# Performance work log

Hardware: AMD Instinct MI355X
Metric: run time of the kernel (lower is better)

The kernel has to match this reference:

```python
import jax, jax.numpy as jnp
import numpy as np

G = 2      # num_generations
B = 16     # meta batch
N = 128    # num_sample
D = 128    # node feature dim (= base_c)
BASE = 128
H = 8      # mha heads
DK = 16    # mha d_k (H*DK = D)
BN_EPS = 1e-5


def setup_inputs() -> dict:
    key = jax.random.key(0)
    ks = jax.random.split(key, 18)

    def nrm(k, shp, s=0.05):
        return jax.random.normal(k, shp, dtype=jnp.float32) * s

    return {
        "vp": jax.random.normal(ks[0], (B, N, D), dtype=jnp.float32),
        "ep": jax.random.uniform(ks[1], (B, N, N), dtype=jnp.float32),
        "ps_w1": nrm(ks[2], (G, 2 * BASE, D)),
        "ps_g1": 1.0 + nrm(ks[3], (G, 2 * BASE), 0.1),
        "ps_b1": nrm(ks[4], (G, 2 * BASE), 0.1),
        "ps_w2": nrm(ks[5], (G, BASE, 2 * BASE)),
        "ps_g2": 1.0 + nrm(ks[6], (G, BASE), 0.1),
        "ps_b2": nrm(ks[7], (G, BASE), 0.1),
        "ps_w3": nrm(ks[8], (G, 1, BASE)),
        "ps_b3": nrm(ks[9], (G, 1), 0.1),
        "d2p_w1": nrm(ks[10], (G, 2 * BASE, 2 * D)),
        "d2p_g1": 1.0 + nrm(ks[11], (G, 2 * BASE), 0.1),
        "d2p_b1": nrm(ks[12], (G, 2 * BASE), 0.1),
        "d2p_w2": nrm(ks[13], (G, BASE, 2 * BASE)),
        "d2p_g2": 1.0 + nrm(ks[14], (G, BASE), 0.1),
        "d2p_b2": nrm(ks[15], (G, BASE), 0.1),
        "wq": nrm(ks[16], (G, H * DK, D)),
        "wk": nrm(ks[17], (G, H * DK, D)),
    }


def _bn(x, g, b):
    # eval-mode BatchNorm with default running stats (mean=0, var=1)
    return x * (g / jnp.sqrt(1.0 + BN_EPS)) + b


def _lrelu(x):
    return jnp.where(x >= 0, x, 0.01 * x)


def _l1norm(x):
    # torch F.normalize(p=1, dim=-1)
    return x / jnp.maximum(jnp.sum(jnp.abs(x), -1, keepdims=True), 1e-12)


def _point_sim(vp, ep, w1, g1, b1, w2, g2, b2, w3, b3, layer):
    # vp: [B,N,D]  ep: [B,N,N]; l2 distance metric
    diff = (vp[:, :, None, :] - vp[:, None, :, :]) ** 2          # [B,N,N,D]
    h = _lrelu(_bn(jnp.einsum('bijd,cd->bijc', diff, w1), g1, b1))  # [B,N,N,2*BASE]
    h = _lrelu(_bn(jnp.einsum('bijc,ec->bije', h, w2), g2, b2))     # [B,N,N,BASE]
    s = jax.nn.sigmoid(jnp.einsum('bije,oe->bijo', h, w3) + b3)[..., 0]  # [B,N,N]
    eye = jnp.eye(N, dtype=vp.dtype)
    ep0 = ep * (1.0 - eye)
    ep_sum = jnp.sum(ep0, -1, keepdims=True)
    e = s * ep0
    if layer > 0:  # PointSimilarity2: top-k sparsify (reproduces torch scatter on dim 1)
        ratio = 0.1 * layer
        kval = int(N * (1.0 - ratio))
        _, idx = jax.lax.top_k(e, kval)                          # [B,N,kval], over dim 2
        bb = jnp.arange(B)[:, None, None]
        kk = jnp.arange(kval)[None, None, :]
        mask = jnp.zeros((B, N, N), dtype=e.dtype).at[bb, idx, kk].set(1.0)
        e = e * mask
    e = _l1norm(e) * ep_sum
    e = e + eye + 1e-6
    e = e / jnp.sum(e, -1, keepdims=True)
    node_sim = -jnp.sum(diff, -1)                                 # [B,N,N]
    return e, node_sim


def _mha_attn(x, wq_g, wk_g):
    # attention-matrix-only MHA; average over heads -> [B,N,N]
    q = (x @ wq_g.T).reshape(B, N, H, DK)
    k = (x @ wk_g.T).reshape(B, N, H, DK)
    logits = jnp.einsum('bihd,bjhd->bhij', q, k) / np.sqrt(DK).astype(np.float32)
    return jnp.mean(jax.nn.softmax(logits, axis=-1), axis=1)


def _d2p(edge, vp, w1, g1, b1, w2, g2, b2):
    eye = jnp.eye(N, dtype=vp.dtype)
    e = _l1norm(edge * (1.0 - eye))
    aggr = jnp.einsum('bij,bjd->bid', e, vp)                      # bmm
    feat = jnp.concatenate([vp, aggr], -1)                        # [B,N,2D]
    h = _lrelu(_bn(feat @ w1.T, g1, b1))
    h = _lrelu(_bn(h @ w2.T, g2, b2))
    return h


def reference(vp, ep, ps_w1, ps_g1, ps_b1, ps_w2, ps_g2, ps_b2, ps_w3, ps_b3,
              d2p_w1, d2p_g1, d2p_b1, d2p_w2, d2p_g2, d2p_b2, wq, wk):
    eps_out, sims_out = [], []
    for g in range(G):
        e, ns = _point_sim(vp, ep, ps_w1[g], ps_g1[g], ps_b1[g], ps_w2[g], ps_g2[g],
                           ps_b2[g], ps_w3[g], ps_b3[g], layer=g)
        attn = _mha_attn(vp, wq[g], wk[g])
        e_fused = 0.5 * (e + attn)
        vp = _d2p(e_fused, vp, d2p_w1[g], d2p_g1[g], d2p_b1[g], d2p_w2[g], d2p_g2[g], d2p_b2[g])
        ep = e
        eps_out.append(e)
        sims_out.append(ns)
    return jnp.stack(eps_out), jnp.stack(sims_out), vp
```

## Files before the change

### kernel.cpp

```cpp
#include <hip/hip_runtime.h>
#include <hip/hip_bf16.h>

typedef unsigned int u32;
typedef unsigned short u16;
typedef float f32x4 __attribute__((ext_vector_type(4)));
typedef float f32x16 __attribute__((ext_vector_type(16)));
typedef short bh8 __attribute__((ext_vector_type(8)));

#define NB 16
#define NN 128
#define DD 128

__device__ __forceinline__ u16 f2bf(float f) {
  union { float f; u32 u; } x; x.f = f;
  u32 r = (x.u + 0x7fffu + ((x.u >> 16) & 1u)) >> 16;
  return (u16)r;
}
__device__ __forceinline__ float bf2f(u16 h) {
  union { u32 u; float f; } x; x.u = ((u32)h) << 16;
  return x.f;
}
__device__ __forceinline__ float lrelu(float x) { return x >= 0.f ? x : 0.01f * x; }
__device__ __forceinline__ f32x16 zero16() {
  f32x16 v;
  #pragma unroll
  for (int r = 0; r < 16; ++r) v[r] = 0.f;
  return v;
}

__global__ void k_pack(const float* __restrict__ ps_w1, const float* __restrict__ ps_w2,
                       const float* __restrict__ d2p_w1, const float* __restrict__ d2p_w2,
                       const float* __restrict__ wq, const float* __restrict__ wk,
                       u16* __restrict__ w1p, u16* __restrict__ w2p,
                       u16* __restrict__ wqA, u16* __restrict__ wkA,
                       u16* __restrict__ w1A, u16* __restrict__ w2A)
{
  int idx = blockIdx.x * 256 + threadIdx.x;
  if (idx < 65536) {
    int r = idx & 7, lane = (idx >> 3) & 63, f = (idx >> 9) & 63, g = idx >> 15;
    int ct = f >> 3, ks = f & 7;
    int c = ct * 32 + (lane & 31), d = ks * 16 + (lane >> 5) * 8 + r;
    w1p[idx] = f2bf(ps_w1[(size_t)g * 32768 + c * 128 + d]);
    return;
  }
  idx -= 65536;
  if (idx < 65536) {
    int r = idx & 7, lane = (idx >> 3) & 63, f = (idx >> 9) & 63, g = idx >> 15;
    int et = f >> 4, ks2 = f & 15;
    int e = et * 32 + (lane & 31), c = ks2 * 16 + (lane >> 5) * 8 + r;
    w2p[idx] = f2bf(ps_w2[(size_t)g * 32768 + e * 256 + c]);
    return;
  }
  idx -= 65536;
  if (idx < 32768) {
    int r = idx & 7, lane = (idx >> 3) & 63, ks = (idx >> 9) & 7, ot = (idx >> 12) & 3, g = idx >> 14;
    int o = ot * 32 + (lane & 31), d = ks * 16 + (lane >> 5) * 8 + r;
    wqA[idx] = f2bf(wq[(size_t)g * 16384 + o * 128 + d]);
    return;
  }
  idx -= 32768;
  if (idx < 32768) {
    int r = idx & 7, lane = (idx >> 3) & 63, ks = (idx >> 9) & 7, ot = (idx >> 12) & 3, g = idx >> 14;
    int o = ot * 32 + (lane & 31), d = ks * 16 + (lane >> 5) * 8 + r;
    wkA[idx] = f2bf(wk[(size_t)g * 16384 + o * 128 + d]);
    return;
  }
  idx -= 32768;
  if (idx < 131072) {
    int r = idx & 7, lane = (idx >> 3) & 63, ks = (idx >> 9) & 15, ot = (idx >> 13) & 7, g = idx >> 16;
    int o = ot * 32 + (lane & 31), q = ks * 16 + (lane >> 5) * 8 + r;
    w1A[idx] = f2bf(d2p_w1[(size_t)g * 65536 + o * 256 + q]);
    return;
  }
  idx -= 131072;
  if (idx < 65536) {
    int r = idx & 7, lane = (idx >> 3) & 63, ks = (idx >> 9) & 15, ot = (idx >> 13) & 3, g = idx >> 15;
    int o = ot * 32 + (lane & 31), q = ks * 16 + (lane >> 5) * 8 + r;
    w2A[idx] = f2bf(d2p_w2[(size_t)g * 32768 + o * 256 + q]);
    return;
  }
}

__global__ __launch_bounds__(256, 2)
void k_point_sim(const float* __restrict__ vp,
                 const u16* __restrict__ w1p, const u16* __restrict__ w2p,
                 const float* __restrict__ g1v, const float* __restrict__ b1v,
                 const float* __restrict__ g2v, const float* __restrict__ b2v,
                 const float* __restrict__ w3v, const float* __restrict__ b3v,
                 float* __restrict__ s_out, float* __restrict__ sims_out)
{
  const int bid = blockIdx.x;
  const int half = bid & 1;
  int rem = (bid >> 1) % 36;
  const int b = (bid >> 1) / 36;
  int ti = 0;
  while (rem >= 8 - ti) { rem -= 8 - ti; ++ti; }
  const int tj = ti + rem;

  const int t = threadIdx.x;
  const int lane = t & 63;
  const int w = t >> 6;
  const int p_l = lane & 31;
  const int hi = lane >> 5;
  const float rsbn = rsqrtf(1.0f + 1e-5f);

  __shared__ u16 Adiff[2][32 * 128];
  __shared__ u16 HL[2][32 * 256];
  __shared__ float sc1[256], bb1[256];
  __shared__ float sc2[128], bb2[128], w3s[128];
  __shared__ float sred[2][4][32];
  __shared__ float simv[128], svv[128];

  sc1[t] = g1v[t] * rsbn; bb1[t] = b1v[t];
  if (t < 128) { sc2[t] = g2v[t] * rsbn; bb2[t] = b2v[t]; w3s[t] = w3v[t]; }

  bh8 a1[2][8];
  #pragma unroll
  for (int c2 = 0; c2 < 2; ++c2)
    #pragma unroll
    for (int ks = 0; ks < 8; ++ks)
      a1[c2][ks] = *(const bh8*)(w1p + (((w * 2 + c2) * 8 + ks) * 64 + lane) * 8);
  bh8 a2[16];
  #pragma unroll
  for (int ks = 0; ks < 16; ++ks)
    a2[ks] = *(const bh8*)(w2p + ((w * 16 + ks) * 64 + lane) * 8);

  const int mtA = half * 4;
  const float* vpb = vp + (size_t)b * NN * DD;

  auto diffgen = [&](int mt, int buf) {
    int p = t >> 3, dseg = t & 7;
    int il = mt * 2 + (p >> 4), jl = p & 15;
    int i = ti * 16 + il, j = tj * 16 + jl;
    const float4* vi = (const float4*)(vpb + i * DD + dseg * 16);
    const float4* vj = (const float4*)(vpb + j * DD + dseg * 16);
    float rs = 0.f;
    u32 pw[8];
    #pragma unroll
    for (int c = 0; c < 4; ++c) {
      float4 av = vi[c], bv = vj[c];
      float d0 = av.x - bv.x; d0 *= d0;
      float d1 = av.y - bv.y; d1 *= d1;
      float d2 = av.z - bv.z; d2 *= d2;
      float d3 = av.w - bv.w; d3 *= d3;
      rs += d0 + d1 + d2 + d3;
      pw[c * 2]     = (u32)f2bf(d0) | ((u32)f2bf(d1) << 16);
      pw[c * 2 + 1] = (u32)f2bf(d2) | ((u32)f2bf(d3) << 16);
    }
    int base = p * 256;
    int off0 = (dseg * 32) ^ ((p & 15) << 4);
    int off1 = (dseg * 32 + 16) ^ ((p & 15) << 4);
    uint4 q0; q0.x = pw[0]; q0.y = pw[1]; q0.z = pw[2]; q0.w = pw[3];
    uint4 q1; q1.x = pw[4]; q1.y = pw[5]; q1.z = pw[6]; q1.w = pw[7];
    *(uint4*)((char*)Adiff[buf] + base + off0) = q0;
    *(uint4*)((char*)Adiff[buf] + base + off1) = q1;
    rs += __shfl_xor(rs, 1);
    rs += __shfl_xor(rs, 2);
    rs += __shfl_xor(rs, 4);
    if ((t & 7) == 0) simv[(mt - mtA) * 32 + p] = rs;
  };

  auto do_l2 = [&](int src) {
    f32x16 acc2 = zero16();
    #pragma unroll
    for (int ks2 = 0; ks2 < 16; ++ks2) {
      int byte = p_l * 512 + ((ks2 * 32 + hi * 16) ^ (p_l << 4));
      bh8 bf = *(const bh8*)((const char*)HL[src] + byte);
      acc2 = __builtin_amdgcn_mfma_f32_32x32x16_bf16(a2[ks2], bf, acc2, 0, 0, 0);
    }
    float psum = 0.f;
    #pragma unroll
    for (int r = 0; r < 16; ++r) {
      int e = w * 32 + (r & 3) + 8 * (r >> 2) + 4 * hi;
      float v = lrelu(acc2[r] * sc2[e] + bb2[e]);
      psum += v * w3s[e];
    }
    psum += __shfl_xor(psum, 32);
    if (hi == 0) sred[src][w][p_l] = psum;
  };

  auto s_final = [&](int ml) {
    if (t < 32) {
      float z = sred[ml & 1][0][t] + sred[ml & 1][1][t] + sred[ml & 1][2][t]
              + sred[ml & 1][3][t] + b3v[0];
      svv[ml * 32 + t] = 1.f / (1.f + __expf(-z));
    }
  };

  diffgen(mtA, 0);
  __syncthreads();

  #pragma unroll
  for (int m = 0; m < 4; ++m) {
    const int cur = m & 1;
    f32x16 acc1[2];
    acc1[0] = zero16(); acc1[1] = zero16();
    #pragma unroll
    for (int ks = 0; ks < 8; ++ks) {
      int byte = p_l * 256 + ((ks * 32 + hi * 16) ^ ((p_l & 15) << 4));
      bh8 bf = *(const bh8*)((const char*)Adiff[cur] + byte);
      acc1[0] = __builtin_amdgcn_mfma_f32_32x32x16_bf16(a1[0][ks], bf, acc1[0], 0, 0, 0);
      acc1[1] = __builtin_amdgcn_mfma_f32_32x32x16_bf16(a1[1][ks], bf, acc1[1], 0, 0, 0);
    }
    if (m < 3) diffgen(mtA + m + 1, cur ^ 1);
    if (m > 0) do_l2(cur ^ 1);
    if (m >= 2) s_final(m - 2);
    #pragma unroll
    for (int c2 = 0; c2 < 2; ++c2) {
      #pragma unroll
      for (int g4 = 0; g4 < 4; ++g4) {
        int c0 = (w * 2 + c2) * 32 + g4 * 8 + hi * 4;
        float v0 = lrelu(acc1[c2][g4 * 4 + 0] * sc1[c0 + 0] + bb1[c0 + 0]);
        float v1 = lrelu(acc1[c2][g4 * 4 + 1] * sc1[c0 + 1] + bb1[c0 + 1]);
        float v2 = lrelu(acc1[c2][g4 * 4 + 2] * sc1[c0 + 2] + bb1[c0 + 2]);
        float v3 = lrelu(acc1[c2][g4 * 4 + 3] * sc1[c0 + 3] + bb1[c0 + 3]);
        uint2 pk;
        pk.x = (u32)f2bf(v0) | ((u32)f2bf(v1) << 16);
        pk.y = (u32)f2bf(v2) | ((u32)f2bf(v3) << 16);
        int byte = p_l * 512 + ((c0 * 2) ^ (p_l << 4));
        *(uint2*)((char*)HL[cur] + byte) = pk;
      }
    }
    __syncthreads();
  }
  do_l2(1);
  s_final(2);
  __syncthreads();
  s_final(3);
  __syncthreads();

  {
    int idx = t & 127;
    int mm = idx >> 5, pp = idx & 31;
    int mt = mtA + mm;
    int i = ti * 16 + mt * 2 + (pp >> 4);
    int j = tj * 16 + (pp & 15);
    float sv = svv[idx];
    float sm = -simv[idx];
    if (t < 128) {
      s_out[(size_t)(b * NN + i) * NN + j] = sv;
      sims_out[(size_t)(b * NN + i) * NN + j] = sm;
    } else if (ti != tj) {
      s_out[(size_t)(b * NN + j) * NN + i] = sv;
      sims_out[(size_t)(b * NN + j) * NN + i] = sm;
    }
  }
}

__global__ void k_rank(const float* __restrict__ s_buf, const float* __restrict__ ep_prev,
                       float* __restrict__ mask)
{
  const int b = blockIdx.x >> 7, n = blockIdx.x & 127, t = threadIdx.x;
  __shared__ float ev[NN];
  size_t row = (size_t)(b * NN + n) * NN;
  float v = s_buf[row + t] * ((t == n) ? 0.f : ep_prev[row + t]);
  ev[t] = v;
  __syncthreads();
  int r = 0;
  for (int j = 0; j < NN; ++j) {
    float vj = ev[j];
    r += (vj > v) || (vj == v && j < t);
  }
  if (r < 115) mask[(size_t)(b * NN + t) * NN + r] = 1.0f;
}

__global__ __launch_bounds__(256)
void k_edge_prep(const float* __restrict__ s_buf, const float* __restrict__ ep_prev,
                 float* __restrict__ maskb, int use_mask, float* __restrict__ eps_out,
                 const float* __restrict__ vp,
                 const u16* __restrict__ wqA, const u16* __restrict__ wkA,
                 u16* __restrict__ Qb, u16* __restrict__ Kb,
                 u16* __restrict__ VPb, u16* __restrict__ VPT)
{
  __shared__ char shm[8448];
  const int t = threadIdx.x;

  if (blockIdx.x < 1024) {
    float* red  = (float*)shm;
    float* red2 = (float*)shm + 8;
    const int rr = t >> 7, tl = t & 127;
    const int rowid = blockIdx.x * 2 + rr;
    const int i = rowid & 127;
    const int wl = (t >> 6) & 1;
    size_t row = (size_t)rowid * 128;
    float ep0 = (tl == i) ? 0.f : ep_prev[row + tl];
    float e = s_buf[row + tl] * ep0;
    if (use_mask) e *= maskb[row + tl];
    else maskb[row + tl] = 0.f;
    float a = ep0, c = fabsf(e);
    #pragma unroll
    for (int o = 32; o; o >>= 1) { a += __shfl_xor(a, o); c += __shfl_xor(c, o); }
    if ((t & 63) == 0) { red[(rr * 2 + wl) * 2 + 0] = a; red[(rr * 2 + wl) * 2 + 1] = c; }
    __syncthreads();
    float epsum = red[(rr * 2) * 2] + red[(rr * 2 + 1) * 2];
    float l1 = red[(rr * 2) * 2 + 1] + red[(rr * 2 + 1) * 2 + 1];
    e = e / fmaxf(l1, 1e-12f) * epsum;
    e += ((tl == i) ? 1.f : 0.f) + 1e-6f;
    float d = e;
    #pragma unroll
    for (int o = 32; o; o >>= 1) d += __shfl_xor(d, o);
    if ((t & 63) == 0) red2[rr * 2 + wl] = d;
    __syncthreads();
    eps_out[row + tl] = e / (red2[rr * 2] + red2[rr * 2 + 1]);
    return;
  }

  u16* VPs = (u16*)shm;
  const int pb = blockIdx.x - 1024;
  const int b = pb >> 2, nt = pb & 3;
  const int w = t >> 6, lane = t & 63, l31 = lane & 31, hi = lane >> 5;
  const float* vpb = vp + (size_t)b * 16384 + (size_t)nt * 32 * 128;

  {
    int r = t >> 3, cseg = t & 7;
    float v[16];
    const float4* src = (const float4*)(vpb + r * 128 + cseg * 16);
    #pragma unroll
    for (int c = 0; c < 4; ++c) {
      float4 a = src[c];
      v[c * 4 + 0] = a.x; v[c * 4 + 1] = a.y; v[c * 4 + 2] = a.z; v[c * 4 + 3] = a.w;
    }
    uint4 pk0, pk1;
    u32* p0 = (u32*)&pk0; u32* p1 = (u32*)&pk1;
    #pragma unroll
    for (int k = 0; k < 4; ++k) {
      p0[k] = (u32)f2bf(v[k * 2 + 0]) | ((u32)f2bf(v[k * 2 + 1]) << 16);
      p1[k] = (u32)f2bf(v[8 + k * 2 + 0]) | ((u32)f2bf(v[8 + k * 2 + 1]) << 16);
    }
    u16* vb = VPb + (size_t)b * 16384 + (nt * 32 + r) * 128 + cseg * 16;
    *(uint4*)(vb) = pk0;
    *(uint4*)(vb + 8) = pk1;
    *(uint4*)((char*)VPs + r * 256 + ((cseg * 32) ^ ((r & 15) << 4))) = pk0;
    *(uint4*)((char*)VPs + r * 256 + ((cseg * 32 + 16) ^ ((r & 15) << 4))) = pk1;
  }
  __syncthreads();

  {
    int col = t >> 1, hh = t & 1;
    u16 tmp[16];
    #pragma unroll
    for (int rr2 = 0; rr2 < 16; ++rr2) {
      int row = hh * 16 + rr2;
      tmp[rr2] = *(const u16*)((char*)VPs + row * 256 + ((col * 2) ^ ((row & 15) << 4)));
    }
    *(uint4*)(VPT + (size_t)b * 16384 + col * 128 + nt * 32 + hh * 16) = *(uint4*)&tmp[0];
    *(uint4*)(VPT + (size_t)b * 16384 + col * 128 + nt * 32 + hh * 16 + 8) = *(uint4*)&tmp[8];
  }

  {
    const int isK = w >> 1;
    const int otp = (w & 1) * 2;
    const u16* wA = isK ? wkA : wqA;
    u16* DST = (isK ? Kb : Qb) + (size_t)b * 16384;
    bh8 bf[8];
    #pragma unroll
    for (int ks = 0; ks < 8; ++ks)
      bf[ks] = *(const bh8*)((char*)VPs + l31 * 256 + (((ks * 32) + hi * 16) ^ ((l31 & 15) << 4)));
    #pragma unroll
    for (int oo = 0; oo < 2; ++oo) {
      int ot = otp + oo;
      f32x16 acc = zero16();
      #pragma unroll
      for (int ks = 0; ks < 8; ++ks) {
        bh8 af = *(const bh8*)(wA + ((size_t)(ot * 8 + ks) * 64 + lane) * 8);
        acc = __builtin_amdgcn_mfma_f32_32x32x16_bf16(af, bf[ks], acc, 0, 0, 0);
      }
      int n = nt * 32 + l31;
      #pragma unroll
      for (int q4 = 0; q4 < 4; ++q4) {
        int o0 = ot * 32 + q4 * 8 + hi * 4;
        uint2 pk;
        pk.x = (u32)f2bf(acc[q4 * 4 + 0]) | ((u32)f2bf(acc[q4 * 4 + 1]) << 16);
        pk.y = (u32)f2bf(acc[q4 * 4 + 2]) | ((u32)f2bf(acc[q4 * 4 + 3]) << 16);
        *(uint2*)(DST + n * 128 + o0) = pk;
      }
    }
  }
}

__global__ __launch_bounds__(256)
void k_attn_d2p(const u16* __restrict__ Qb, const u16* __restrict__ Kb,
                const float* __restrict__ eps_g,
                const u16* __restrict__ VPb, const u16* __restrict__ VPT,
                const u16* __restrict__ w1A, const float* __restrict__ g1v, const float* __restrict__ b1v,
                const u16* __restrict__ w2A, const float* __restrict__ g2v, const float* __restrict__ b2v,
                float* __restrict__ vpn)
{
  __shared__ char shm[40960];
  u16* att  = (u16*)shm;
  u16* AG   = (u16*)shm;
  u16* HB   = (u16*)(shm + 8192);
  u16* EFNl = (u16*)(shm + 32768);

  const int b = blockIdx.x >> 2;
  const int ch = blockIdx.x & 3;
  const int t = threadIdx.x;
  const int w = t >> 6;
  const int lane = t & 63;
  const int l31 = lane & 31;
  const int hi = lane >> 5;
  const float rsbn = rsqrtf(1.f + 1e-5f);

  {
    float asum[64];
    #pragma unroll
    for (int z = 0; z < 64; ++z) asum[z] = 0.f;
    const u16* Qrow = Qb + (size_t)b * 16384 + (ch * 32 + l31) * 128;
    #pragma unroll
    for (int hh = 0; hh < 2; ++hh) {
      int h = w * 2 + hh;
      bh8 qf = *(const bh8*)(Qrow + h * 16 + hi * 8);
      f32x16 lg[4];
      #pragma unroll
      for (int jt = 0; jt < 4; ++jt) {
        bh8 kf = *(const bh8*)(Kb + (size_t)b * 16384 + (jt * 32 + l31) * 128 + h * 16 + hi * 8);
        f32x16 zz = zero16();
        lg[jt] = __builtin_amdgcn_mfma_f32_32x32x16_bf16(kf, qf, zz, 0, 0, 0);
      }
      float m = lg[0][0];
      #pragma unroll
      for (int jt = 0; jt < 4; ++jt)
        #pragma unroll
        for (int r = 0; r < 16; ++r) m = fmaxf(m, lg[jt][r]);
      m = fmaxf(m, __shfl_xor(m, 32));
      float sum = 0.f;
      #pragma unroll
      for (int jt = 0; jt < 4; ++jt)
        #pragma unroll
        for (int r = 0; r < 16; ++r) {
          float e = __expf((lg[jt][r] - m) * 0.25f);
          lg[jt][r] = e;
          sum += e;
        }
      sum += __shfl_xor(sum, 32);
      float inv = 1.f / sum;
      #pragma unroll
      for (int jt = 0; jt < 4; ++jt)
        #pragma unroll
        for (int r = 0; r < 16; ++r) asum[jt * 16 + r] += lg[jt][r] * inv;
    }
    #pragma unroll
    for (int jt = 0; jt < 4; ++jt)
      #pragma unroll
      for (int q4 = 0; q4 < 4; ++q4) {
        int j0 = jt * 32 + q4 * 8 + hi * 4;
        uint2 pk;
        pk.x = (u32)f2bf(asum[jt * 16 + q4 * 4 + 0]) | ((u32)f2bf(asum[jt * 16 + q4 * 4 + 1]) << 16);
        pk.y = (u32)f2bf(asum[jt * 16 + q4 * 4 + 2]) | ((u32)f2bf(asum[jt * 16 + q4 * 4 + 3]) << 16);
        *(uint2*)((char*)att + (w * 32 + l31) * 256 + ((j0 * 2) ^ ((l31 & 15) << 4))) = pk;
      }
  }
  __syncthreads();

  {
    int il = t >> 3, jseg = t & 7;
    int i = ch * 32 + il;
    float a[16];
    #pragma unroll
    for (int z = 0; z < 16; ++z) a[z] = 0.f;
    #pragma unroll
    for (int ww = 0; ww < 4; ++ww) {
      #pragma unroll
      for (int c = 0; c < 2; ++c) {
        uint4 v = *(const uint4*)((char*)att + (ww * 32 + il) * 256 + (((jseg * 32) + c * 16) ^ ((il & 15) << 4)));
        u32 uu[4] = {v.x, v.y, v.z, v.w};
        #pragma unroll
        for (int k = 0; k < 4; ++k) {
          a[c * 8 + k * 2 + 0] += bf2f((u16)(uu[k] & 0xffff));
          a[c * 8 + k * 2 + 1] += bf2f((u16)(uu[k] >> 16));
        }
      }
    }
    const float* erow = eps_g + ((size_t)b * 128 + i) * 128 + jseg * 16;
    float f[16];
    float s = 0.f;
    #pragma unroll
    for (int c = 0; c < 4; ++c) {
      float4 ev = *(const float4*)(erow + c * 4);
      float evs[4] = {ev.x, ev.y, ev.z, ev.w};
      #pragma unroll
      for (int k = 0; k < 4; ++k) {
        int jj = jseg * 16 + c * 4 + k;
        float fv = 0.5f * (evs[k] + a[c * 4 + k] * 0.125f);
        if (jj == i) fv = 0.f;
        f[c * 4 + k] = fv;
        s += fabsf(fv);
      }
    }
    s += __shfl_xor(s, 1);
    s += __shfl_xor(s, 2);
    s += __shfl_xor(s, 4);
    float inv = 1.f / fmaxf(s, 1e-12f);
    uint4 o0, o1;
    u32* op = (u32*)&o0;
    u32* op1 = (u32*)&o1;
    #pragma unroll
    for (int k = 0; k < 4; ++k) {
      op[k]  = (u32)f2bf(f[k * 2 + 0] * inv) | ((u32)f2bf(f[k * 2 + 1] * inv) << 16);
      op1[k] = (u32)f2bf(f[8 + k * 2 + 0] * inv) | ((u32)f2bf(f[8 + k * 2 + 1] * inv) << 16);
    }
    __syncthreads();
    *(uint4*)((char*)EFNl + il * 256 + ((jseg * 32) ^ ((il & 15) << 4))) = o0;
    *(uint4*)((char*)EFNl + il * 256 + ((jseg * 32 + 16) ^ ((il & 15) << 4))) = o1;
  }
  __syncthreads();

  {
    const u16* vtrow = VPT + (size_t)b * 16384 + (w * 32 + l31) * 128;
    f32x16 acc = zero16();
    #pragma unroll
    for (int ks = 0; ks < 8; ++ks) {
      bh8 af = *(const bh8*)(vtrow + ks * 16 + hi * 8);
      bh8 bf = *(const bh8*)((char*)EFNl + l31 * 256 + (((ks * 32) + hi * 16) ^ ((l31 & 15) << 4)));
      acc = __builtin_amdgcn_mfma_f32_32x32x16_bf16(af, bf, acc, 0, 0, 0);
    }
    #pragma unroll
    for (int q4 = 0; q4 < 4; ++q4) {
      int d0 = w * 32 + q4 * 8 + hi * 4;
      uint2 pk;
      pk.x = (u32)f2bf(acc[q4 * 4 + 0]) | ((u32)f2bf(acc[q4 * 4 + 1]) << 16);
      pk.y = (u32)f2bf(acc[q4 * 4 + 2]) | ((u32)f2bf(acc[q4 * 4 + 3]) << 16);
      *(uint2*)((char*)AG + l31 * 256 + ((d0 * 2) ^ ((l31 & 15) << 4))) = pk;
    }
  }
  __syncthreads();

  {
    const u16* vprow = VPb + (size_t)b * 16384 + (ch * 32 + l31) * 128;
    f32x16 acc0 = zero16(), acc1v = zero16();
    #pragma unroll
    for (int ks = 0; ks < 16; ++ks) {
      bh8 a0 = *(const bh8*)(w1A + ((size_t)((w * 2 + 0) * 16 + ks)) * 512 + lane * 8);
      bh8 a1 = *(const bh8*)(w1A + ((size_t)((w * 2 + 1) * 16 + ks)) * 512 + lane * 8);
      bh8 bf;
      if (ks < 8) bf = *(const bh8*)(vprow + ks * 16 + hi * 8);
      else bf = *(const bh8*)((char*)AG + l31 * 256 + ((((ks - 8) * 32) + hi * 16) ^ ((l31 & 15) << 4)));
      acc0 = __builtin_amdgcn_mfma_f32_32x32x16_bf16(a0, bf, acc0, 0, 0, 0);
      acc1v = __builtin_amdgcn_mfma_f32_32x32x16_bf16(a1, bf, acc1v, 0, 0, 0);
    }
    #pragma unroll
    for (int oo = 0; oo < 2; ++oo) {
      const f32x16& acc = oo ? acc1v : acc0;
      #pragma unroll
      for (int q4 = 0; q4 < 4; ++q4) {
        int o0 = (w * 2 + oo) * 32 + q4 * 8 + hi * 4;
        float4 gg = *(const float4*)(g1v + o0);
        float4 bb = *(const float4*)(b1v + o0);
        float v0 = lrelu(acc[q4 * 4 + 0] * (gg.x * rsbn) + bb.x);
        float v1 = lrelu(acc[q4 * 4 + 1] * (gg.y * rsbn) + bb.y);
        float v2 = lrelu(acc[q4 * 4 + 2] * (gg.z * rsbn) + bb.z);
        float v3 = lrelu(acc[q4 * 4 + 3] * (gg.w * rsbn) + bb.w);
        uint2 pk;
        pk.x = (u32)f2bf(v0) | ((u32)f2bf(v1) << 16);
        pk.y = (u32)f2bf(v2) | ((u32)f2bf(v3) << 16);
        *(uint2*)((char*)HB + l31 * 512 + ((o0 * 2) ^ (l31 << 4))) = pk;
      }
    }
  }
  __syncthreads();

  {
    f32x16 acc = zero16();
    #pragma unroll
    for (int ks = 0; ks < 16; ++ks) {
      bh8 af = *(const bh8*)(w2A + ((size_t)(w * 16 + ks)) * 512 + lane * 8);
      bh8 bf = *(const bh8*)((char*)HB + l31 * 512 + (((ks * 32) + hi * 16) ^ (l31 << 4)));
      acc = __builtin_amdgcn_mfma_f32_32x32x16_bf16(af, bf, acc, 0, 0, 0);
    }
    int i = ch * 32 + l31;
    #pragma unroll
    for (int q4 = 0; q4 < 4; ++q4) {
      int o0 = w * 32 + q4 * 8 + hi * 4;
      float4 gg = *(const float4*)(g2v + o0);
      float4 bb = *(const float4*)(b2v + o0);
      float4 ov;
      ov.x = lrelu(acc[q4 * 4 + 0] * (gg.x * rsbn) + bb.x);
      ov.y = lrelu(acc[q4 * 4 + 1] * (gg.y * rsbn) + bb.y);
      ov.z = lrelu(acc[q4 * 4 + 2] * (gg.z * rsbn) + bb.z);
      ov.w = lrelu(acc[q4 * 4 + 3] * (gg.w * rsbn) + bb.w);
      *(float4*)(vpn + ((size_t)b * 128 + i) * 128 + o0) = ov;
    }
  }
}

extern "C" void kernel_launch(void* const* d_in, const int* in_sizes, int n_in,
                              void* d_out, int out_size, void* d_ws, size_t ws_size,
                              hipStream_t stream)
{
  (void)in_sizes; (void)n_in; (void)out_size; (void)ws_size;
  const float* vp_in  = (const float*)d_in[0];
  const float* ep_in  = (const float*)d_in[1];
  const float* ps_w1  = (const float*)d_in[2];
  const float* ps_g1  = (const float*)d_in[3];
  const float* ps_b1  = (const float*)d_in[4];
  const float* ps_w2  = (const float*)d_in[5];
  const float* ps_g2  = (const float*)d_in[6];
  const float* ps_b2  = (const float*)d_in[7];
  const float* ps_w3  = (const float*)d_in[8];
  const float* ps_b3  = (const float*)d_in[9];
  const float* d2p_w1 = (const float*)d_in[10];
  const float* d2p_g1 = (const float*)d_in[11];
  const float* d2p_b1 = (const float*)d_in[12];
  const float* d2p_w2 = (const float*)d_in[13];
  const float* d2p_g2 = (const float*)d_in[14];
  const float* d2p_b2 = (const float*)d_in[15];
  const float* wq     = (const float*)d_in[16];
  const float* wk     = (const float*)d_in[17];

  float* out = (float*)d_out;
  float* eps_base  = out;
  float* sims_base = out + 524288;
  float* vp_out    = out + 1048576;

  char* ws = (char*)d_ws;
  float* s_buf = (float*)(ws + ((size_t)0 << 20));
  float* maskb = (float*)(ws + ((size_t)1 << 20));
  float* vp1   = (float*)(ws + ((size_t)2 << 20));
  u16* Qb   = (u16*)(ws + ((size_t)3 << 20));
  u16* Kb   = (u16*)(ws + ((size_t)3 << 20) + 524288);
  u16* VPb  = (u16*)(ws + ((size_t)4 << 20));
  u16* VPT  = (u16*)(ws + ((size_t)4 << 20) + 524288);
  u16* w1p  = (u16*)(ws + ((size_t)5 << 20));
  u16* w2p  = w1p + 65536;
  u16* wqA  = w2p + 65536;
  u16* wkA  = wqA + 32768;
  u16* w1A  = wkA + 32768;
  u16* w2A  = w1A + 131072;

  k_pack<<<dim3(1536), 256, 0, stream>>>(ps_w1, ps_w2, d2p_w1, d2p_w2, wq, wk,
                                         w1p, w2p, wqA, wkA, w1A, w2A);

  for (int g = 0; g < 2; ++g) {
    const float* vpc = g ? (const float*)vp1 : vp_in;
    float* vpn = g ? vp_out : vp1;
    float* eps_g  = eps_base + (size_t)g * 262144;
    float* sims_g = sims_base + (size_t)g * 262144;
    const float* epprev = g ? eps_base : ep_in;

    k_point_sim<<<dim3(1152), 256, 0, stream>>>(vpc,
        w1p + (size_t)g * 32768, w2p + (size_t)g * 32768,
        ps_g1 + g * 256, ps_b1 + g * 256,
        ps_g2 + g * 128, ps_b2 + g * 128,
        ps_w3 + g * 128, ps_b3 + g, s_buf, sims_g);
    if (g) k_rank<<<dim3(2048), 128, 0, stream>>>(s_buf, epprev, maskb);
    k_edge_prep<<<dim3(1088), 256, 0, stream>>>(s_buf, epprev, maskb, g, eps_g,
        vpc, wqA + (size_t)g * 16384, wkA + (size_t)g * 16384, Qb, Kb, VPb, VPT);
    k_attn_d2p<<<dim3(64), 256, 0, stream>>>(Qb, Kb, eps_g, VPb, VPT,
        w1A + (size_t)g * 65536, d2p_g1 + g * 256, d2p_b1 + g * 256,
        w2A + (size_t)g * 32768, d2p_g2 + g * 128, d2p_b2 + g * 128, vpn);
  }
}
```

Measured before the change: 135.7 us.

## Use hardware bf16 pack conversion, branchless lrelu, direct output stores, higher occupancy

Replaces the software round-to-nearest bf16 packing with the v_cvt_pk_bf16_f32 instruction in every kernel, and rewrites leaky ReLU as a max. This cuts ALU work in the epilogues. In the point-similarity kernel the staging arrays for sims and sigmoid outputs are removed: values are written straight to global memory, which drops a barrier and some LDS use. The launch bound is raised to three blocks per CU, which may force register spills given the large A-fragment register cache.

```diff
diff --git a/kernel.cpp b/kernel.cpp
--- a/kernel.cpp
+++ b/kernel.cpp
@@ -16,11 +16,16 @@
   u32 r = (x.u + 0x7fffu + ((x.u >> 16) & 1u)) >> 16;
   return (u16)r;
 }
+__device__ __forceinline__ u32 cvtpk(float lo, float hi) {
+  u32 r;
+  asm("v_cvt_pk_bf16_f32 %0, %1, %2" : "=v"(r) : "v"(lo), "v"(hi));
+  return r;
+}
 __device__ __forceinline__ float bf2f(u16 h) {
   union { u32 u; float f; } x; x.u = ((u32)h) << 16;
   return x.f;
 }
-__device__ __forceinline__ float lrelu(float x) { return x >= 0.f ? x : 0.01f * x; }
+__device__ __forceinline__ float lrelu(float x) { return fmaxf(x, 0.01f * x); }
 __device__ __forceinline__ f32x16 zero16() {
   f32x16 v;
   #pragma unroll
@@ -81,7 +86,7 @@
   }
 }
 
-__global__ __launch_bounds__(256, 2)
+__global__ __launch_bounds__(256, 3)
 void k_point_sim(const float* __restrict__ vp,
                  const u16* __restrict__ w1p, const u16* __restrict__ w2p,
                  const float* __restrict__ g1v, const float* __restrict__ b1v,
@@ -109,7 +114,6 @@
   __shared__ float sc1[256], bb1[256];
   __shared__ float sc2[128], bb2[128], w3s[128];
   __shared__ float sred[2][4][32];
-  __shared__ float simv[128], svv[128];
 
   sc1[t] = g1v[t] * rsbn; bb1[t] = b1v[t];
   if (t < 128) { sc2[t] = g2v[t] * rsbn; bb2[t] = b2v[t]; w3s[t] = w3v[t]; }
@@ -144,8 +148,8 @@
       float d2 = av.z - bv.z; d2 *= d2;
       float d3 = av.w - bv.w; d3 *= d3;
       rs += d0 + d1 + d2 + d3;
-      pw[c * 2]     = (u32)f2bf(d0) | ((u32)f2bf(d1) << 16);
-      pw[c * 2 + 1] = (u32)f2bf(d2) | ((u32)f2bf(d3) << 16);
+      pw[c * 2]     = cvtpk(d0, d1);
+      pw[c * 2 + 1] = cvtpk(d2, d3);
     }
     int base = p * 256;
     int off0 = (dseg * 32) ^ ((p & 15) << 4);
@@ -157,7 +161,10 @@
     rs += __shfl_xor(rs, 1);
     rs += __shfl_xor(rs, 2);
     rs += __shfl_xor(rs, 4);
-    if ((t & 7) == 0) simv[(mt - mtA) * 32 + p] = rs;
+    if ((t & 7) == 0) {
+      sims_out[(size_t)(b * NN + i) * NN + j] = -rs;
+      if (ti != tj) sims_out[(size_t)(b * NN + j) * NN + i] = -rs;
+    }
   };
 
   auto do_l2 = [&](int src) {
@@ -183,7 +190,12 @@
     if (t < 32) {
       float z = sred[ml & 1][0][t] + sred[ml & 1][1][t] + sred[ml & 1][2][t]
               + sred[ml & 1][3][t] + b3v[0];
-      svv[ml * 32 + t] = 1.f / (1.f + __expf(-z));
+      float sv = 1.f / (1.f + __expf(-z));
+      int mt = mtA + ml;
+      int i = ti * 16 + mt * 2 + (t >> 4);
+      int j = tj * 16 + (t & 15);
+      s_out[(size_t)(b * NN + i) * NN + j] = sv;
+      if (ti != tj) s_out[(size_t)(b * NN + j) * NN + i] = sv;
     }
   };
 
@@ -215,8 +227,8 @@
         float v2 = lrelu(acc1[c2][g4 * 4 + 2] * sc1[c0 + 2] + bb1[c0 + 2]);
         float v3 = lrelu(acc1[c2][g4 * 4 + 3] * sc1[c0 + 3] + bb1[c0 + 3]);
         uint2 pk;
-        pk.x = (u32)f2bf(v0) | ((u32)f2bf(v1) << 16);
-        pk.y = (u32)f2bf(v2) | ((u32)f2bf(v3) << 16);
+        pk.x = cvtpk(v0, v1);
+        pk.y = cvtpk(v2, v3);
         int byte = p_l * 512 + ((c0 * 2) ^ (p_l << 4));
         *(uint2*)((char*)HL[cur] + byte) = pk;
       }
@@ -227,24 +239,6 @@
   s_final(2);
   __syncthreads();
   s_final(3);
-  __syncthreads();
-
-  {
-    int idx = t & 127;
-    int mm = idx >> 5, pp = idx & 31;
-    int mt = mtA + mm;
-    int i = ti * 16 + mt * 2 + (pp >> 4);
-    int j = tj * 16 + (pp & 15);
-    float sv = svv[idx];
-    float sm = -simv[idx];
-    if (t < 128) {
-      s_out[(size_t)(b * NN + i) * NN + j] = sv;
-      sims_out[(size_t)(b * NN + i) * NN + j] = sm;
-    } else if (ti != tj) {
-      s_out[(size_t)(b * NN + j) * NN + i] = sv;
-      sims_out[(size_t)(b * NN + j) * NN + i] = sm;
-    }
-  }
 }
 
 __global__ void k_rank(const float* __restrict__ s_buf, const float* __restrict__ ep_prev,
@@ -324,8 +318,8 @@
     u32* p0 = (u32*)&pk0; u32* p1 = (u32*)&pk1;
     #pragma unroll
     for (int k = 0; k < 4; ++k) {
-      p0[k] = (u32)f2bf(v[k * 2 + 0]) | ((u32)f2bf(v[k * 2 + 1]) << 16);
-      p1[k] = (u32)f2bf(v[8 + k * 2 + 0]) | ((u32)f2bf(v[8 + k * 2 + 1]) << 16);
+      p0[k] = cvtpk(v[k * 2 + 0], v[k * 2 + 1]);
+      p1[k] = cvtpk(v[8 + k * 2 + 0], v[8 + k * 2 + 1]);
     }
     u16* vb = VPb + (size_t)b * 16384 + (nt * 32 + r) * 128 + cseg * 16;
     *(uint4*)(vb) = pk0;
@@ -370,8 +364,8 @@
       for (int q4 = 0; q4 < 4; ++q4) {
         int o0 = ot * 32 + q4 * 8 + hi * 4;
         uint2 pk;
-        pk.x = (u32)f2bf(acc[q4 * 4 + 0]) | ((u32)f2bf(acc[q4 * 4 + 1]) << 16);
-        pk.y = (u32)f2bf(acc[q4 * 4 + 2]) | ((u32)f2bf(acc[q4 * 4 + 3]) << 16);
+        pk.x = cvtpk(acc[q4 * 4 + 0], acc[q4 * 4 + 1]);
+        pk.y = cvtpk(acc[q4 * 4 + 2], acc[q4 * 4 + 3]);
         *(uint2*)(DST + n * 128 + o0) = pk;
       }
     }
@@ -445,8 +439,8 @@
       for (int q4 = 0; q4 < 4; ++q4) {
         int j0 = jt * 32 + q4 * 8 + hi * 4;
         uint2 pk;
-        pk.x = (u32)f2bf(asum[jt * 16 + q4 * 4 + 0]) | ((u32)f2bf(asum[jt * 16 + q4 * 4 + 1]) << 16);
-        pk.y = (u32)f2bf(asum[jt * 16 + q4 * 4 + 2]) | ((u32)f2bf(asum[jt * 16 + q4 * 4 + 3]) << 16);
+        pk.x = cvtpk(asum[jt * 16 + q4 * 4 + 0], asum[jt * 16 + q4 * 4 + 1]);
+        pk.y = cvtpk(asum[jt * 16 + q4 * 4 + 2], asum[jt * 16 + q4 * 4 + 3]);
         *(uint2*)((char*)att + (w * 32 + l31) * 256 + ((j0 * 2) ^ ((l31 & 15) << 4))) = pk;
       }
   }
@@ -496,8 +490,8 @@
     u32* op1 = (u32*)&o1;
     #pragma unroll
     for (int k = 0; k < 4; ++k) {
-      op[k]  = (u32)f2bf(f[k * 2 + 0] * inv) | ((u32)f2bf(f[k * 2 + 1] * inv) << 16);
-      op1[k] = (u32)f2bf(f[8 + k * 2 + 0] * inv) | ((u32)f2bf(f[8 + k * 2 + 1] * inv) << 16);
+      op[k]  = cvtpk(f[k * 2 + 0] * inv, f[k * 2 + 1] * inv);
+      op1[k] = cvtpk(f[8 + k * 2 + 0] * inv, f[8 + k * 2 + 1] * inv);
     }
     __syncthreads();
     *(uint4*)((char*)EFNl + il * 256 + ((jseg * 32) ^ ((il & 15) << 4))) = o0;
@@ -518,8 +512,8 @@
     for (int q4 = 0; q4 < 4; ++q4) {
       int d0 = w * 32 + q4 * 8 + hi * 4;
       uint2 pk;
-      pk.x = (u32)f2bf(acc[q4 * 4 + 0]) | ((u32)f2bf(acc[q4 * 4 + 1]) << 16);
-      pk.y = (u32)f2bf(acc[q4 * 4 + 2]) | ((u32)f2bf(acc[q4 * 4 + 3]) << 16);
+      pk.x = cvtpk(acc[q4 * 4 + 0], acc[q4 * 4 + 1]);
+      pk.y = cvtpk(acc[q4 * 4 + 2], acc[q4 * 4 + 3]);
       *(uint2*)((char*)AG + l31 * 256 + ((d0 * 2) ^ ((l31 & 15) << 4))) = pk;
     }
   }
@@ -551,8 +545,8 @@
         float v2 = lrelu(acc[q4 * 4 + 2] * (gg.z * rsbn) + bb.z);
         float v3 = lrelu(acc[q4 * 4 + 3] * (gg.w * rsbn) + bb.w);
         uint2 pk;
-        pk.x = (u32)f2bf(v0) | ((u32)f2bf(v1) << 16);
-        pk.y = (u32)f2bf(v2) | ((u32)f2bf(v3) << 16);
+        pk.x = cvtpk(v0, v1);
+        pk.y = cvtpk(v2, v3);
         *(uint2*)((char*)HB + l31 * 512 + ((o0 * 2) ^ (l31 << 4))) = pk;
       }
     }
```

New measurement: 242.8 us. 78.9% more time.
